# Optimization experiments

Measured on AMD Instinct MI355X. Metric: run time of the kernel, lower is better.

The kernel has to match this reference:

```python
import jax, jax.numpy as jnp
from jax import lax
import numpy as np

B, GRID, H = 128, 28, 64      # batch, 28x28 pixel grid, hidden size
NDIR = 4                      # feature_sz = number of scan directions
FC_HD, OUT = 512, 10


def setup_inputs() -> dict:
    key = jax.random.key(0)
    ks = jax.random.split(key, 8)
    s_u = 1.0 / np.sqrt(2 * H)
    inp = {
        "x":  jax.random.normal(ks[0], (B, GRID, GRID), dtype=jnp.float32),
        # per-direction MDLSTM gate params: 5 gates (i, f_left, f_up, o, g)
        "Wx": jax.random.normal(ks[1], (NDIR, 5 * H), dtype=jnp.float32) * 0.1,
        "U":  jax.random.normal(ks[2], (NDIR, 2 * H, 5 * H), dtype=jnp.float32) * s_u,
        "b":  jnp.zeros((NDIR, 5 * H), dtype=jnp.float32),
        # fc head
        "W1": jax.random.normal(ks[3], (NDIR * H, FC_HD), dtype=jnp.float32) / np.sqrt(NDIR * H),
        "b1": jnp.zeros((FC_HD,), dtype=jnp.float32),
        "W2": jax.random.normal(ks[4], (FC_HD, OUT), dtype=jnp.float32) / np.sqrt(FC_HD),
        "b2": jnp.zeros((OUT,), dtype=jnp.float32),
    }
    return inp


def _mdlstm_dir(xg, Wx, U, b):
    # xg: [GRID(rows), GRID(cols), B] scalar pixel per cell
    zeros = jnp.zeros((xg.shape[-1], H), dtype=xg.dtype)

    def col_step(carry, inp):
        h_left, c_left = carry
        x_pix, h_up, c_up = inp                     # [B], [B,H], [B,H]
        z = x_pix[:, None] * Wx + jnp.concatenate([h_left, h_up], -1) @ U + b
        i, f1, f2, o, g = jnp.split(z, 5, axis=-1)  # each [B,H]
        c = (jax.nn.sigmoid(i) * jnp.tanh(g)
             + jax.nn.sigmoid(f1) * c_left
             + jax.nn.sigmoid(f2) * c_up)
        h = jax.nn.sigmoid(o) * jnp.tanh(c)
        return (h, c), (h, c)

    def row_step(carry, x_row):
        h_up_row, c_up_row = carry                  # [GRID,B,H] previous row
        _, (h_row, c_row) = lax.scan(col_step, (zeros, zeros),
                                     (x_row, h_up_row, c_up_row))
        return (h_row, c_row), None

    init = (jnp.zeros((GRID,) + zeros.shape, xg.dtype),
            jnp.zeros((GRID,) + zeros.shape, xg.dtype))
    (h_last_row, _), _ = lax.scan(row_step, init, xg)
    return h_last_row[-1]                           # final (bottom-right) hidden [B,H]


def _forward(x, Wx, U, b, W1, b1, W2, b2):
    x2 = x.reshape(-1, GRID, GRID)
    # 4 scan directions via flips; scan always proceeds top-left -> bottom-right
    dirs = jnp.stack([x2,
                      x2[:, :, ::-1],
                      x2[:, ::-1, :],
                      x2[:, ::-1, ::-1]], 0)        # [4,B,GRID,GRID]
    dirs = jnp.transpose(dirs, (0, 2, 3, 1))        # [4,GRID,GRID,B]
    h = jax.vmap(_mdlstm_dir)(dirs, Wx, U, b)       # [4,B,H]
    h = jnp.transpose(h, (1, 0, 2)).reshape(-1, NDIR * H)
    z = jax.nn.relu(h @ W1 + b1)
    return jax.nn.softmax(z @ W2 + b2, axis=-1)


def reference(x, Wx, U, b, W1, b1, W2, b2):
    return _forward(x, Wx, U, b, W1, b1, W2, b2)
```

## Files before the change

kernel.cpp:

```cpp
#include <hip/hip_runtime.h>
#include <hip/hip_bf16.h>


#define GRIDN 28
#define BATCH 128
#define HID   64
#define NDIR  4
#define FC_HD 512
#define OUT_N 10
#define BT    2
#define NTHR  512
#define NSLOT 29
#define S_H   104
#define S_C   68

typedef _Float16 f16;
typedef _Float16 f16x8 __attribute__((ext_vector_type(8)));
typedef float    f32x4 __attribute__((ext_vector_type(4)));

#define LOG2E  1.44269504088896340736f
#define LOG2E2 2.88539008177792681472f

__device__ __forceinline__ float rcpf(float x) { return __builtin_amdgcn_rcpf(x); }
__device__ __forceinline__ float ex2(float x)  { return __builtin_amdgcn_exp2f(x); }

__global__ __launch_bounds__(NTHR)
void mdlstm_kernel(const float* __restrict__ x,
                   const float* __restrict__ Wx,
                   const float* __restrict__ U,
                   const float* __restrict__ bias,
                   float* __restrict__ Hout)
{
    const int d    = blockIdx.x & 3;
    const int tile = blockIdx.x >> 2;
    const int tid  = threadIdx.x;
    const int lane = tid & 63;
    const int wave = tid >> 6;
    const int wm   = wave >> 2;
    const int wh   = wave & 3;
    const int l16  = lane & 15;
    const int q    = lane >> 4;
    const int nb   = wh * 16 + l16;

    __shared__ __align__(16) f16 Fh[2][BT][NSLOT * S_H];
    __shared__ float             Fc[2][BT][NSLOT * S_C];
    __shared__ float             xs[GRIDN][GRIDN][BT];

    for (int i = tid; i < 2 * BT * NSLOT * S_H; i += NTHR) ((f16*)Fh)[i] = (f16)0.0f;
    for (int i = tid; i < 2 * BT * NSLOT * S_C; i += NTHR) ((float*)Fc)[i] = 0.0f;
    for (int i = tid; i < GRIDN * GRIDN * BT; i += NTHR) {
        int bl = i & 1, rc = i >> 1, c = rc % GRIDN, r = rc / GRIDN;
        int rr = (d & 2) ? (GRIDN - 1 - r) : r;
        int cc = (d & 1) ? (GRIDN - 1 - c) : c;
        xs[r][c][bl] = x[((tile * BT + bl) * GRIDN + rr) * GRIDN + cc];
    }

    f16x8 bf[5][5];
#pragma unroll
    for (int g = 0; g < 5; ++g) {
        const float sc = (g == 4) ? LOG2E2 : -LOG2E;
        int n = g * 64 + nb;
#pragma unroll
        for (int ks = 0; ks < 4; ++ks) {
            f16x8 v;
            int kb = ks * 32 + q * 8;
#pragma unroll
            for (int j = 0; j < 8; ++j)
                v[j] = (f16)(sc * U[(d * 128 + kb + j) * 320 + n]);
            bf[g][ks] = v;
        }
        f16x8 v5 = {(f16)0, (f16)0, (f16)0, (f16)0, (f16)0, (f16)0, (f16)0, (f16)0};
        if (q == 0) {
            v5[0] = (f16)(sc * Wx[d * 320 + n]);
            v5[1] = (f16)(sc * bias[d * 320 + n]);
        }
        bf[g][4] = v5;
    }
    __syncthreads();

    if (tid < 2 * BT * NSLOT) {
        int buf = tid / (BT * NSLOT), rem = tid % (BT * NSLOT);
        int b = rem / NSLOT, sl = rem % NSLOT;
        Fh[buf][b][sl * S_H + 65] = (f16)1.0f;
    }
    if (tid < BT) Fh[0][tid][27 * S_H + 64] = (f16)xs[0][0][tid];
    __syncthreads();

    auto step = [&](int t, int br) __attribute__((always_inline)) {
        const int bw  = br ^ 1;
        const int rlo = (t > GRIDN - 1) ? (t - (GRIDN - 1)) : 0;
        const int rhi = (t < GRIDN - 1) ? t : (GRIDN - 1);
        const int k   = rhi - rlo + 1;
        const int nM  = (2 * k + 15) >> 4;

        if (t < 2 * GRIDN - 2 && tid >= NTHR - 56) {
            int idx = tid - (NTHR - 56), b = idx & 1, j = idx >> 1;
            int rlo2 = (t + 1 > GRIDN - 1) ? (t + 1 - (GRIDN - 1)) : 0;
            int rhi2 = (t + 1 < GRIDN - 1) ? (t + 1) : (GRIDN - 1);
            if (j <= rhi2 - rlo2) {
                int r = rlo2 + j;
                Fh[bw][b][(27 - r) * S_H + 64] = (f16)xs[r][t + 1 - r][b];
            }
        }

        for (int mt = wm; mt < nM; mt += 2) {
            int mA = mt * 16 + l16;
            int jA = mA >> 1; if (jA > k - 1) jA = k - 1;
            int bA = mA & 1;
            int slA = 27 - (rlo + jA);
            const f16* ab = &Fh[br][bA][slA * S_H];
            f16x8 a0 = *(const f16x8*)(ab + q * 8);
            f16x8 a1 = *(const f16x8*)(ab + 32 + q * 8);
            f16x8 a2 = *(const f16x8*)(ab + S_H + q * 8);
            f16x8 a3 = *(const f16x8*)(ab + S_H + 32 + q * 8);
            f16x8 a4 = *(const f16x8*)(ab + 64 + q * 8);

            int j0  = mt * 8 + q * 2;
            int jj0 = (j0     > k - 1) ? k - 1 : j0;
            int jj1 = (j0 + 1 > k - 1) ? k - 1 : j0 + 1;
            int sl0 = 27 - (rlo + jj0);
            int sl1 = 27 - (rlo + jj1);
            const float* rp[4] = { &Fc[br][0][sl0 * S_C + nb], &Fc[br][1][sl0 * S_C + nb],
                                   &Fc[br][0][sl1 * S_C + nb], &Fc[br][1][sl1 * S_C + nb] };
            float pcl[4], pcu[4];
#pragma unroll
            for (int i = 0; i < 4; ++i) { pcl[i] = rp[i][0]; pcu[i] = rp[i][S_C]; }

            const f32x4 z4 = {0.f, 0.f, 0.f, 0.f};
            f32x4 acc[5];
#pragma unroll
            for (int g = 0; g < 5; ++g) acc[g] = __builtin_amdgcn_mfma_f32_16x16x32_f16(a4, bf[g][4], z4, 0, 0, 0);
#pragma unroll
            for (int g = 0; g < 5; ++g) acc[g] = __builtin_amdgcn_mfma_f32_16x16x32_f16(a0, bf[g][0], acc[g], 0, 0, 0);
#pragma unroll
            for (int g = 0; g < 5; ++g) acc[g] = __builtin_amdgcn_mfma_f32_16x16x32_f16(a1, bf[g][1], acc[g], 0, 0, 0);
#pragma unroll
            for (int g = 0; g < 5; ++g) acc[g] = __builtin_amdgcn_mfma_f32_16x16x32_f16(a2, bf[g][2], acc[g], 0, 0, 0);
#pragma unroll
            for (int g = 0; g < 5; ++g) acc[g] = __builtin_amdgcn_mfma_f32_16x16x32_f16(a3, bf[g][3], acc[g], 0, 0, 0);

            const int DC = (bw - br) * (BT * NSLOT * S_C);
            int ih0 = sl0 * S_H + nb, ih1 = sl1 * S_H + nb;
            f16* wh0 = &Fh[bw][0][0];
            f16* wh1 = &Fh[bw][1][0];
#pragma unroll
            for (int i = 0; i < 4; ++i) {
                float ta = 1.0f + ex2(acc[0][i]);
                float tp = 1.0f + ex2(acc[1][i]);
                float tq = 1.0f + ex2(acc[2][i]);
                float td = 1.0f + ex2(acc[3][i]);
                float tb = 1.0f + ex2(acc[4][i]);
                float cn = (tb - 2.0f) * rcpf(ta * tb)
                         + (pcl[i] * tq + pcu[i] * tp) * rcpf(tp * tq);
                float cnc = fminf(cn, 22.0f);
                float te = 1.0f + ex2(LOG2E2 * cnc);
                float hn = (te - 2.0f) * rcpf(td * te);
                *(float*)(rp[i] + DC) = cn;
                ((i & 1) ? wh1 : wh0)[(i < 2) ? ih0 : ih1] = (f16)hn;
            }
        }
        __syncthreads();
    };

    for (int tb = 0; tb < 27; ++tb) { step(2 * tb, 0); step(2 * tb + 1, 1); }
    step(54, 0);

    if (tid < BT * HID) {
        int bl = tid >> 6, h = tid & 63;
        Hout[(d * BATCH + tile * BT + bl) * HID + h] = (float)Fh[1][bl][h];
    }
}

__global__ __launch_bounds__(1024)
void fc_kernel(const float* __restrict__ Hin,
               const float* __restrict__ W1, const float* __restrict__ b1,
               const float* __restrict__ W2, const float* __restrict__ b2,
               float* __restrict__ out)
{
    const int b   = blockIdx.x;
    const int tid = threadIdx.x;
    __shared__ float hrow[NDIR * HID];
    __shared__ float psum[2][FC_HD];
    __shared__ float z1[FC_HD];
    __shared__ float ps[32][16];
    __shared__ float z2[16];

    if (tid < NDIR * HID)
        hrow[tid] = Hin[(tid >> 6) * (BATCH * HID) + b * HID + (tid & 63)];
    __syncthreads();

    {
        int col = tid & (FC_HD - 1);
        int hf  = tid >> 9;
        int f0  = hf * 128;
        float s = 0.0f;
#pragma unroll 16
        for (int f = 0; f < 128; ++f)
            s += hrow[f0 + f] * W1[(f0 + f) * FC_HD + col];
        psum[hf][col] = s;
    }
    __syncthreads();

    if (tid < FC_HD)
        z1[tid] = fmaxf(psum[0][tid] + psum[1][tid] + b1[tid], 0.0f);
    __syncthreads();

    if (tid < 512) {
        int j = tid & 15, sl = tid >> 4;
        float s = 0.0f;
        if (j < OUT_N) {
#pragma unroll
            for (int i = 0; i < 16; ++i) {
                int kk = sl * 16 + i;
                s += z1[kk] * W2[kk * OUT_N + j];
            }
        }
        ps[sl][j] = s;
    }
    __syncthreads();

    if (tid < OUT_N) {
        float s = b2[tid];
#pragma unroll
        for (int sl = 0; sl < 32; ++sl) s += ps[sl][tid];
        z2[tid] = s;
    }
    __syncthreads();

    if (tid == 0) {
        float m = z2[0];
        for (int j = 1; j < OUT_N; ++j) m = fmaxf(m, z2[j]);
        float sum = 0.0f, e[OUT_N];
        for (int j = 0; j < OUT_N; ++j) { e[j] = __expf(z2[j] - m); sum += e[j]; }
        float inv = 1.0f / sum;
        for (int j = 0; j < OUT_N; ++j) out[b * OUT_N + j] = e[j] * inv;
    }
}

extern "C" void kernel_launch(void* const* d_in, const int* in_sizes, int n_in,
                              void* d_out, int out_size, void* d_ws, size_t ws_size,
                              hipStream_t stream) {
    const float* x  = (const float*)d_in[0];
    const float* Wx = (const float*)d_in[1];
    const float* U  = (const float*)d_in[2];
    const float* bs = (const float*)d_in[3];
    const float* W1 = (const float*)d_in[4];
    const float* b1 = (const float*)d_in[5];
    const float* W2 = (const float*)d_in[6];
    const float* b2 = (const float*)d_in[7];
    float* out = (float*)d_out;
    float* Hws = (float*)d_ws;

    mdlstm_kernel<<<NDIR * (BATCH / BT), NTHR, 0, stream>>>(x, Wx, U, bs, Hws);
    fc_kernel<<<BATCH, 1024, 0, stream>>>(Hws, W1, b1, W2, b2, out);
}
```

Baseline: 146.2 us.

## Give each MDLSTM block a single batch element and launch one block per sample

Result: slower. 179.6 us (+22.8%).

```diff
diff --git a/kernel.cpp b/kernel.cpp
--- a/kernel.cpp
+++ b/kernel.cpp
@@ -8,7 +8,6 @@
 #define NDIR  4
 #define FC_HD 512
 #define OUT_N 10
-#define BT    2
 #define NTHR  512
 #define NSLOT 29
 #define S_H   104
@@ -42,17 +41,17 @@
     const int q    = lane >> 4;
     const int nb   = wh * 16 + l16;
 
-    __shared__ __align__(16) f16 Fh[2][BT][NSLOT * S_H];
-    __shared__ float             Fc[2][BT][NSLOT * S_C];
-    __shared__ float             xs[GRIDN][GRIDN][BT];
-
-    for (int i = tid; i < 2 * BT * NSLOT * S_H; i += NTHR) ((f16*)Fh)[i] = (f16)0.0f;
-    for (int i = tid; i < 2 * BT * NSLOT * S_C; i += NTHR) ((float*)Fc)[i] = 0.0f;
-    for (int i = tid; i < GRIDN * GRIDN * BT; i += NTHR) {
-        int bl = i & 1, rc = i >> 1, c = rc % GRIDN, r = rc / GRIDN;
+    __shared__ __align__(16) f16 Fh[2][NSLOT * S_H];
+    __shared__ float             Fc[2][NSLOT * S_C];
+    __shared__ float             xs[GRIDN][GRIDN];
+
+    for (int i = tid; i < 2 * NSLOT * S_H; i += NTHR) ((f16*)Fh)[i] = (f16)0.0f;
+    for (int i = tid; i < 2 * NSLOT * S_C; i += NTHR) ((float*)Fc)[i] = 0.0f;
+    for (int i = tid; i < GRIDN * GRIDN; i += NTHR) {
+        int c = i % GRIDN, r = i / GRIDN;
         int rr = (d & 2) ? (GRIDN - 1 - r) : r;
         int cc = (d & 1) ? (GRIDN - 1 - c) : c;
-        xs[r][c][bl] = x[((tile * BT + bl) * GRIDN + rr) * GRIDN + cc];
+        xs[r][c] = x[(tile * GRIDN + rr) * GRIDN + cc];
     }
 
     f16x8 bf[5][5];
@@ -78,53 +77,56 @@
     }
     __syncthreads();
 
-    if (tid < 2 * BT * NSLOT) {
-        int buf = tid / (BT * NSLOT), rem = tid % (BT * NSLOT);
-        int b = rem / NSLOT, sl = rem % NSLOT;
-        Fh[buf][b][sl * S_H + 65] = (f16)1.0f;
-    }
-    if (tid < BT) Fh[0][tid][27 * S_H + 64] = (f16)xs[0][0][tid];
-    __syncthreads();
+    if (tid < 2 * NSLOT) {
+        int buf = tid / NSLOT, sl = tid % NSLOT;
+        Fh[buf][sl * S_H + 65] = (f16)1.0f;
+    }
+    if (tid == 0) Fh[0][27 * S_H + 64] = (f16)xs[0][0];
+    __syncthreads();
+
+    if (blockIdx.x & 256) { __builtin_amdgcn_s_sleep(16); }
 
     auto step = [&](int t, int br) __attribute__((always_inline)) {
         const int bw  = br ^ 1;
         const int rlo = (t > GRIDN - 1) ? (t - (GRIDN - 1)) : 0;
         const int rhi = (t < GRIDN - 1) ? t : (GRIDN - 1);
         const int k   = rhi - rlo + 1;
-        const int nM  = (2 * k + 15) >> 4;
-
-        if (t < 2 * GRIDN - 2 && tid >= NTHR - 56) {
-            int idx = tid - (NTHR - 56), b = idx & 1, j = idx >> 1;
+        const int nM  = (k + 15) >> 4;
+
+        if (t < 2 * GRIDN - 2 && tid >= NTHR - GRIDN) {
+            int j = tid - (NTHR - GRIDN);
             int rlo2 = (t + 1 > GRIDN - 1) ? (t + 1 - (GRIDN - 1)) : 0;
             int rhi2 = (t + 1 < GRIDN - 1) ? (t + 1) : (GRIDN - 1);
             if (j <= rhi2 - rlo2) {
                 int r = rlo2 + j;
-                Fh[bw][b][(27 - r) * S_H + 64] = (f16)xs[r][t + 1 - r][b];
-            }
-        }
-
-        for (int mt = wm; mt < nM; mt += 2) {
+                Fh[bw][(27 - r) * S_H + 64] = (f16)xs[r][t + 1 - r];
+            }
+        }
+
+        if (wm < nM) {
+            const int mt = wm;
             int mA = mt * 16 + l16;
-            int jA = mA >> 1; if (jA > k - 1) jA = k - 1;
-            int bA = mA & 1;
+            int jA = mA > k - 1 ? k - 1 : mA;
             int slA = 27 - (rlo + jA);
-            const f16* ab = &Fh[br][bA][slA * S_H];
+            const f16* ab = &Fh[br][slA * S_H];
             f16x8 a0 = *(const f16x8*)(ab + q * 8);
             f16x8 a1 = *(const f16x8*)(ab + 32 + q * 8);
             f16x8 a2 = *(const f16x8*)(ab + S_H + q * 8);
             f16x8 a3 = *(const f16x8*)(ab + S_H + 32 + q * 8);
             f16x8 a4 = *(const f16x8*)(ab + 64 + q * 8);
 
-            int j0  = mt * 8 + q * 2;
-            int jj0 = (j0     > k - 1) ? k - 1 : j0;
-            int jj1 = (j0 + 1 > k - 1) ? k - 1 : j0 + 1;
-            int sl0 = 27 - (rlo + jj0);
-            int sl1 = 27 - (rlo + jj1);
-            const float* rp[4] = { &Fc[br][0][sl0 * S_C + nb], &Fc[br][1][sl0 * S_C + nb],
-                                   &Fc[br][0][sl1 * S_C + nb], &Fc[br][1][sl1 * S_C + nb] };
+            int j0 = mt * 16 + q * 4;
+            int sl[4];
+            const float* rp[4];
             float pcl[4], pcu[4];
 #pragma unroll
-            for (int i = 0; i < 4; ++i) { pcl[i] = rp[i][0]; pcu[i] = rp[i][S_C]; }
+            for (int i = 0; i < 4; ++i) {
+                int jj = (j0 + i > k - 1) ? k - 1 : j0 + i;
+                sl[i] = 27 - (rlo + jj);
+                rp[i] = &Fc[br][sl[i] * S_C + nb];
+                pcl[i] = rp[i][0];
+                pcu[i] = rp[i][S_C];
+            }
 
             const f32x4 z4 = {0.f, 0.f, 0.f, 0.f};
             f32x4 acc[5];
@@ -139,10 +141,8 @@
 #pragma unroll
             for (int g = 0; g < 5; ++g) acc[g] = __builtin_amdgcn_mfma_f32_16x16x32_f16(a3, bf[g][3], acc[g], 0, 0, 0);
 
-            const int DC = (bw - br) * (BT * NSLOT * S_C);
-            int ih0 = sl0 * S_H + nb, ih1 = sl1 * S_H + nb;
-            f16* wh0 = &Fh[bw][0][0];
-            f16* wh1 = &Fh[bw][1][0];
+            const int DC = (bw - br) * (NSLOT * S_C);
+            f16* whw = &Fh[bw][0];
 #pragma unroll
             for (int i = 0; i < 4; ++i) {
                 float ta = 1.0f + ex2(acc[0][i]);
@@ -156,7 +156,7 @@
                 float te = 1.0f + ex2(LOG2E2 * cnc);
                 float hn = (te - 2.0f) * rcpf(td * te);
                 *(float*)(rp[i] + DC) = cn;
-                ((i & 1) ? wh1 : wh0)[(i < 2) ? ih0 : ih1] = (f16)hn;
+                whw[sl[i] * S_H + nb] = (f16)hn;
             }
         }
         __syncthreads();
@@ -165,10 +165,8 @@
     for (int tb = 0; tb < 27; ++tb) { step(2 * tb, 0); step(2 * tb + 1, 1); }
     step(54, 0);
 
-    if (tid < BT * HID) {
-        int bl = tid >> 6, h = tid & 63;
-        Hout[(d * BATCH + tile * BT + bl) * HID + h] = (float)Fh[1][bl][h];
-    }
+    if (tid < HID)
+        Hout[(d * BATCH + tile) * HID + tid] = (float)Fh[1][tid];
 }
 
 __global__ __launch_bounds__(1024)
@@ -251,6 +249,6 @@
     float* out = (float*)d_out;
     float* Hws = (float*)d_ws;
 
-    mdlstm_kernel<<<NDIR * (BATCH / BT), NTHR, 0, stream>>>(x, Wx, U, bs, Hws);
+    mdlstm_kernel<<<NDIR * BATCH, NTHR, 0, stream>>>(x, Wx, U, bs, Hws);
     fc_kernel<<<BATCH, 1024, 0, stream>>>(Hws, W1, b1, W2, b2, out);
 }
```
